# Optimization experiments

Measured on AMD Instinct MI355X. Metric: run time of the kernel, lower is better.

Reference implementation:

```python
import jax, jax.numpy as jnp
import numpy as np

I, H, B, T = 17, 128, 32768, 19

def setup_inputs() -> dict:
    key = jax.random.key(0)
    ks = jax.random.split(key, 7)
    s = 1.0 / np.sqrt(H)  # PyTorch LSTMCell/Linear init scale
    u = lambda k, shape: jax.random.uniform(k, shape, jnp.float32, -s, s)
    return {
        "x": jax.random.normal(ks[0], (B, T, I), jnp.float32),
        "W_ih": u(ks[1], (4 * H, I)),
        "W_hh": u(ks[2], (4 * H, H)),
        "b_ih": u(ks[3], (4 * H,)),
        "b_hh": u(ks[4], (4 * H,)),
        "W_out": u(ks[5], (I, H)),
        "b_out": u(ks[6], (I,)),
    }

def reference(x, W_ih, W_hh, b_ih, b_hh, W_out, b_out):
    B_, T_, _ = x.shape
    Hh = W_hh.shape[1]
    # Precompute input projections for all timesteps in one GEMM: [B,T,4H]
    x_proj = jnp.einsum('bti,gi->btg', x, W_ih) + b_ih + b_hh

    def step(carry, xp_t):
        h, c = carry
        gates = xp_t + h @ W_hh.T            # [B,4H]
        i_g, f_g, g_g, o_g = jnp.split(gates, 4, axis=-1)
        c = jax.nn.sigmoid(f_g) * c + jax.nn.sigmoid(i_g) * jnp.tanh(g_g)
        h = jax.nn.sigmoid(o_g) * jnp.tanh(c)
        y = h @ W_out.T + b_out              # [B,I]
        return (h, c), y

    h0 = jnp.zeros((B_, Hh), x.dtype)
    c0 = jnp.zeros((B_, Hh), x.dtype)
    _, ys = jax.lax.scan(step, (h0, c0), jnp.swapaxes(x_proj, 0, 1))  # ys: [T,B,I]
    return jnp.swapaxes(ys, 0, 1)  # [B,T,I]
```

## Files before the change

kernel.cpp:

```cpp
#include <hip/hip_runtime.h>

#define I_DIM 17
#define H_DIM 128
#define T_DIM 19
#define B_DIM 32768
#define M_ROWS 128
#define NTHR 512
#define GRID (B_DIM / M_ROWS)
#define XI 323
#define NF (M_ROWS * XI)
#define XSLOT 4352

#define OFF_H 0
#define OFF_X 65536
#define OFF_WO 148224
#define LDS_TOT 156416

typedef __bf16 bf16x8 __attribute__((ext_vector_type(8)));
typedef float f32x4 __attribute__((ext_vector_type(4)));
typedef float f32x4u __attribute__((ext_vector_type(4), aligned(4)));
union FragU { bf16x8 v; unsigned short s[8]; uint4 u; };

#define K1 1.4426950408889634f
#define K2 2.8853900817779268f

__device__ __forceinline__ unsigned short f2bf(float f) {
    union { float f; unsigned u; } x; x.f = f;
    return (unsigned short)((x.u + 0x8000u) >> 16);
}

#define SGB_STEP() do {                                        \
    _Pragma("unroll")                                          \
    for (int it_ = 0; it_ < 32; ++it_) {                       \
        __builtin_amdgcn_sched_group_barrier(0x100, 2, 0);     \
        __builtin_amdgcn_sched_group_barrier(0x008, 5, 0);     \
        __builtin_amdgcn_sched_group_barrier(0x002, 18, 0);    \
    }                                                          \
} while (0)

#define MFMA_Q(P_, QT_, ACC_, REC_) do {                                          \
    _Pragma("unroll") for (int m2 = 0; m2 < 2; ++m2) {                            \
        _Pragma("unroll") for (int g = 0; g < 4; ++g)                             \
            ACC_[m2][g] = bias[g];                                                \
        FragU fx; fx.u = (uint4){0u, 0u, 0u, 0u};                                 \
        if (q < 2)                                                                \
            fx.v = *(const bf16x8*)(smem + xyA + ((QT_) * 2 + m2) * 512);         \
        else if (q == 2)                                                          \
            fx.s[0] = *(const unsigned short*)(smem + xk16 + ((QT_) * 2 + m2) * 32); \
        _Pragma("unroll") for (int g = 0; g < 4; ++g)                             \
            ACC_[m2][g] = __builtin_amdgcn_mfma_f32_16x16x32_bf16(wihr[g], fx.v, ACC_[m2][g], 0, 0, 0); \
    }                                                                             \
    if (REC_) {                                                                   \
        _Pragma("unroll") for (int kk = 0; kk < 4; ++kk)                          \
            _Pragma("unroll") for (int m2 = 0; m2 < 2; ++m2) {                    \
                bf16x8 a = *(const bf16x8*)(smem + vkk[kk] + ((1 - (P_)) * 32768 + ((QT_) * 2 + m2) * 4096)); \
                _Pragma("unroll") for (int g = 0; g < 4; ++g)                     \
                    ACC_[m2][g] = __builtin_amdgcn_mfma_f32_16x16x32_bf16(whh[kk][g], a, ACC_[m2][g], 0, 0, 0); \
            }                                                                     \
    }                                                                             \
} while (0)

#define ELEM_Q(P_, QT_, ACC_) do {                                                \
    _Pragma("unroll") for (int m2 = 0; m2 < 2; ++m2) {                            \
        unsigned long long hp = 0ull;                                             \
        _Pragma("unroll") for (int r = 0; r < 4; ++r) {                           \
            float ui = __builtin_amdgcn_exp2f(ACC_[m2][0][r]);                    \
            float uf = __builtin_amdgcn_exp2f(ACC_[m2][1][r]);                    \
            float vg = __builtin_amdgcn_exp2f(ACC_[m2][2][r]);                    \
            float uo = __builtin_amdgcn_exp2f(ACC_[m2][3][r]);                    \
            float A_ = 1.f + ui, F_ = 1.f + uf, G_ = 1.f + vg;                    \
            float AG = A_ * G_;                                                   \
            int ci = (QT_) * 8 + m2 * 4 + r;                                      \
            float c = (cst[ci] * AG + (1.f - vg) * F_) * __builtin_amdgcn_rcpf(F_ * AG); \
            cst[ci] = c;                                                          \
            float vc = __builtin_amdgcn_exp2f(-K2 * c);                           \
            float h = (1.f - vc) * __builtin_amdgcn_rcpf((1.f + uo) * (1.f + vc));\
            union { float f; unsigned u; } hu; hu.f = h;                          \
            hp |= (unsigned long long)((hu.u + 0x8000u) >> 16) << (16 * r);       \
        }                                                                         \
        *(unsigned long long*)(smem + vwrT + ((P_) * 32768 + ((QT_) * 2 + m2) * 4096)) = hp; \
    }                                                                             \
} while (0)

#define Y_BURST(P_) do {                                                          \
    f32x4 ya0 = {0.f, 0.f, 0.f, 0.f}, ya1 = {0.f, 0.f, 0.f, 0.f};                 \
    _Pragma("unroll") for (int kk = 0; kk < 4; ++kk) {                            \
        bf16x8 wa = *(const bf16x8*)(smem + vwo + kk * 1024);                     \
        bf16x8 h0 = *(const bf16x8*)(smem + vkk[kk] + yrt + (1 - (P_)) * 32768);  \
        bf16x8 h1 = *(const bf16x8*)(smem + vkk[kk] + yrt + 4096 + (1 - (P_)) * 32768); \
        ya0 = __builtin_amdgcn_mfma_f32_16x16x32_bf16(wa, h0, ya0, 0, 0, 0);      \
        ya1 = __builtin_amdgcn_mfma_f32_16x16x32_bf16(wa, h1, ya1, 0, 0, 0);      \
    }                                                                             \
    if (yct == 0) {                                                               \
        *(f32x4u*)ypt0 = ya0 + ybo;                                               \
        *(f32x4u*)ypt1 = ya1 + ybo;                                               \
    } else if (q == 0) {                                                          \
        ypt0[0] = ya0[0] + ybo[0];                                                \
        ypt1[0] = ya1[0] + ybo[0];                                                \
    }                                                                             \
    ypt0 += I_DIM; ypt1 += I_DIM;                                                 \
} while (0)

#define STEP(P_) do {                      \
    MFMA_Q(P_, 0, accA, 1);                \
    MFMA_Q(P_, 1, accB, 1);                \
    ELEM_Q(P_, 0, accA);                   \
    MFMA_Q(P_, 2, accA, 1);                \
    ELEM_Q(P_, 1, accB);                   \
    MFMA_Q(P_, 3, accB, 1);                \
    ELEM_Q(P_, 2, accA);                   \
    Y_BURST(P_);                           \
    ELEM_Q(P_, 3, accB);                   \
    xyA += XSLOT; xk16 += XSLOT;           \
    SGB_STEP();                            \
    __syncthreads();                       \
} while (0)

__global__ __launch_bounds__(NTHR)
__attribute__((amdgpu_waves_per_eu(2, 2)))
void flowlstm(
    const float* __restrict__ x, const float* __restrict__ W_ih,
    const float* __restrict__ W_hh, const float* __restrict__ b_ih,
    const float* __restrict__ b_hh, const float* __restrict__ W_out,
    const float* __restrict__ b_out, float* __restrict__ out)
{
    __shared__ __align__(16) unsigned char smem[LDS_TOT];
    const int tid = threadIdx.x;
    const int w = tid >> 6, lane = tid & 63, l15 = lane & 15, q = lane >> 4;
    const int cg = w;
    const int b0 = blockIdx.x * M_ROWS;

    {
        const float* xb = x + (size_t)b0 * XI;
        for (int j = 0; j < 81; ++j) {
            int f = tid + j * NTHR;
            if (f < NF) {
                float v = xb[f];
                unsigned uf_ = (unsigned)f;
                unsigned row = (uf_ * 51943u) >> 24;
                unsigned s = uf_ - row * 323u;
                unsigned t = (s * 61681u) >> 20;
                unsigned k = s - t * 17u;
                unsigned a;
                if (k == 16) a = OFF_X + t * XSLOT + 4096 + row * 2;
                else a = OFF_X + t * XSLOT + (row >> 4) * 512 + (k >> 3) * 256
                       + (row & 15) * 16 + (k & 7) * 2;
                *(unsigned short*)(smem + a) = f2bf(v);
            }
        }
    }
    {
        int ln = tid & 63, f = tid >> 6;
        int kk = f & 3, ct = f >> 2;
        int o = ct * 16 + (ln & 15);
        int kb = kk * 32 + (ln >> 4) * 8;
        FragU fu;
        #pragma unroll
        for (int e = 0; e < 8; ++e)
            fu.s[e] = (o < I_DIM) ? f2bf(W_out[o * H_DIM + kb + e]) : (unsigned short)0;
        *(uint4*)(smem + OFF_WO + f * 1024 + ln * 16) = fu.u;
    }
    float gsc[4] = { -K1, -K1, -K2, -K1 };

    bf16x8 whh[4][4];
    #pragma unroll
    for (int kk = 0; kk < 4; ++kk)
        #pragma unroll
        for (int g = 0; g < 4; ++g) {
            int n = g * H_DIM + cg * 16 + l15;
            const float* s = W_hh + n * H_DIM + kk * 32 + q * 8;
            FragU fu;
            #pragma unroll
            for (int e = 0; e < 8; ++e) fu.s[e] = f2bf(s[e] * gsc[g]);
            whh[kk][g] = fu.v;
        }
    bf16x8 wihr[4];
    #pragma unroll
    for (int g = 0; g < 4; ++g) {
        int n = g * H_DIM + cg * 16 + l15;
        FragU fu;
        #pragma unroll
        for (int e = 0; e < 8; ++e) {
            int k = q * 8 + e;
            fu.s[e] = (k < I_DIM) ? f2bf(W_ih[n * I_DIM + k] * gsc[g]) : (unsigned short)0;
        }
        wihr[g] = fu.v;
    }
    f32x4 bias[4];
    #pragma unroll
    for (int g = 0; g < 4; ++g)
        #pragma unroll
        for (int r = 0; r < 4; ++r) {
            int col = g * H_DIM + cg * 16 + 4 * q + r;
            bias[g][r] = (b_ih[col] + b_hh[col]) * gsc[g];
        }
    const unsigned xr7 = (unsigned)((l15 & 7) << 4);
    unsigned vkk[4];
    #pragma unroll
    for (int kk = 0; kk < 4; ++kk)
        vkk[kk] = (unsigned)(l15 * 256 + ((kk * 64 + q * 16) ^ xr7));
    const unsigned vwrT = (unsigned)(l15 * 256 + (((cg * 16 + 4 * q) * 2) ^ xr7));
    const int yct = w & 1;
    const unsigned yrt = (unsigned)((w >> 1) * 8192);
    const unsigned vwo = (unsigned)(OFF_WO + yct * 4096 + lane * 16);
    f32x4 ybo;
    #pragma unroll
    for (int r = 0; r < 4; ++r) {
        int col = yct * 16 + 4 * q + r;
        ybo[r] = b_out[col < I_DIM ? col : 16];
    }
    unsigned xyA  = (unsigned)(OFF_X + (q < 2 ? q * 256 : 0) + l15 * 16);
    unsigned xk16 = (unsigned)(OFF_X + 4096 + l15 * 2);
    float* ypt0 = out + (size_t)(b0 + (w >> 1) * 32 + l15) * XI + (yct ? 16 : 4 * q);
    float* ypt1 = ypt0 + (size_t)16 * XI;

    float cst[32];
    #pragma unroll
    for (int i = 0; i < 32; ++i) cst[i] = 0.f;

    f32x4 accA[2][4], accB[2][4];

    __syncthreads();

    MFMA_Q(0, 0, accA, 0);
    MFMA_Q(0, 1, accB, 0);
    ELEM_Q(0, 0, accA);
    MFMA_Q(0, 2, accA, 0);
    ELEM_Q(0, 1, accB);
    MFMA_Q(0, 3, accB, 0);
    ELEM_Q(0, 2, accA);
    ELEM_Q(0, 3, accB);
    xyA += XSLOT; xk16 += XSLOT;
    __syncthreads();

    #pragma unroll 1
    for (int t = 1; t < T_DIM; t += 2) {
        STEP(1);
        STEP(0);
    }

    {
        f32x4 ya0 = {0.f, 0.f, 0.f, 0.f}, ya1 = {0.f, 0.f, 0.f, 0.f};
        #pragma unroll
        for (int kk = 0; kk < 4; ++kk) {
            bf16x8 wa = *(const bf16x8*)(smem + vwo + kk * 1024);
            bf16x8 h0 = *(const bf16x8*)(smem + vkk[kk] + yrt);
            bf16x8 h1 = *(const bf16x8*)(smem + vkk[kk] + yrt + 4096);
            ya0 = __builtin_amdgcn_mfma_f32_16x16x32_bf16(wa, h0, ya0, 0, 0, 0);
            ya1 = __builtin_amdgcn_mfma_f32_16x16x32_bf16(wa, h1, ya1, 0, 0, 0);
        }
        if (yct == 0) {
            *(f32x4u*)ypt0 = ya0 + ybo;
            *(f32x4u*)ypt1 = ya1 + ybo;
        } else if (q == 0) {
            ypt0[0] = ya0[0] + ybo[0];
            ypt1[0] = ya1[0] + ybo[0];
        }
    }
}

extern "C" void kernel_launch(void* const* d_in, const int* in_sizes, int n_in,
                              void* d_out, int out_size, void* d_ws, size_t ws_size,
                              hipStream_t stream) {
    const float* x     = (const float*)d_in[0];
    const float* W_ih  = (const float*)d_in[1];
    const float* W_hh  = (const float*)d_in[2];
    const float* b_ih  = (const float*)d_in[3];
    const float* b_hh  = (const float*)d_in[4];
    const float* W_out = (const float*)d_in[5];
    const float* b_out = (const float*)d_in[6];
    float* out = (float*)d_out;

    dim3 grid(GRID), block(NTHR);
    flowlstm<<<grid, block, 0, stream>>>(x, W_ih, W_hh, b_ih, b_hh, W_out, b_out, out);
}
```

Measured before the change: 150.0 us.

## Split batch tile into two half-groups and ping-pong LSTM steps between them

Splits the 128-row block into two 64-row groups with separate h buffers in LDS (GB0/GB1) and interleaves them: while one group's elementwise gate math runs, the other group's MFMA recurrence is issued. This replaces double-buffering h over time, which shrinks the LDS footprint, and drops the explicit sched_group_barrier scheduling hints. The intent is to overlap the transcendental VALU work with matrix-core work across independent batch halves. The cost is two barriers per timestep instead of one, and instruction ordering now depends on the compiler's default scheduling.

```diff
diff --git a/kernel.cpp b/kernel.cpp
--- a/kernel.cpp
+++ b/kernel.cpp
@@ -11,10 +11,11 @@
 #define NF (M_ROWS * XI)
 #define XSLOT 4352
 
-#define OFF_H 0
-#define OFF_X 65536
-#define OFF_WO 148224
-#define LDS_TOT 156416
+#define GB0 0
+#define GB1 16384
+#define OFF_X 32768
+#define OFF_WO 115456
+#define LDS_TOT 123648
 
 typedef __bf16 bf16x8 __attribute__((ext_vector_type(8)));
 typedef float f32x4 __attribute__((ext_vector_type(4)));
@@ -29,91 +30,57 @@
     return (unsigned short)((x.u + 0x8000u) >> 16);
 }
 
-#define SGB_STEP() do {                                        \
-    _Pragma("unroll")                                          \
-    for (int it_ = 0; it_ < 32; ++it_) {                       \
-        __builtin_amdgcn_sched_group_barrier(0x100, 2, 0);     \
-        __builtin_amdgcn_sched_group_barrier(0x008, 5, 0);     \
-        __builtin_amdgcn_sched_group_barrier(0x002, 18, 0);    \
-    }                                                          \
+#define MFMA_Q(QT_, GB_, XB_, XK_, REC_) do {                                     \
+    _Pragma("unroll") for (int g = 0; g < 4; ++g)                                 \
+        acc[QT_][g] = bias[g];                                                    \
+    FragU fx; fx.u = (uint4){0u, 0u, 0u, 0u};                                     \
+    if (q < 2)                                                                    \
+        fx.v = *(const bf16x8*)(smem + (XB_) + (QT_) * 512);                      \
+    else if (q == 2)                                                              \
+        fx.s[0] = *(const unsigned short*)(smem + (XK_) + (QT_) * 32);            \
+    _Pragma("unroll") for (int g = 0; g < 4; ++g)                                 \
+        acc[QT_][g] = __builtin_amdgcn_mfma_f32_16x16x32_bf16(wihr[g], fx.v, acc[QT_][g], 0, 0, 0); \
+    if (REC_) {                                                                   \
+        _Pragma("unroll") for (int kk = 0; kk < 4; ++kk) {                        \
+            bf16x8 a = *(const bf16x8*)(smem + vkk[kk] + ((GB_) + (QT_) * 4096)); \
+            _Pragma("unroll") for (int g = 0; g < 4; ++g)                         \
+                acc[QT_][g] = __builtin_amdgcn_mfma_f32_16x16x32_bf16(whh[kk][g], a, acc[QT_][g], 0, 0, 0); \
+        }                                                                         \
+    }                                                                             \
 } while (0)
 
-#define MFMA_Q(P_, QT_, ACC_, REC_) do {                                          \
-    _Pragma("unroll") for (int m2 = 0; m2 < 2; ++m2) {                            \
-        _Pragma("unroll") for (int g = 0; g < 4; ++g)                             \
-            ACC_[m2][g] = bias[g];                                                \
-        FragU fx; fx.u = (uint4){0u, 0u, 0u, 0u};                                 \
-        if (q < 2)                                                                \
-            fx.v = *(const bf16x8*)(smem + xyA + ((QT_) * 2 + m2) * 512);         \
-        else if (q == 2)                                                          \
-            fx.s[0] = *(const unsigned short*)(smem + xk16 + ((QT_) * 2 + m2) * 32); \
-        _Pragma("unroll") for (int g = 0; g < 4; ++g)                             \
-            ACC_[m2][g] = __builtin_amdgcn_mfma_f32_16x16x32_bf16(wihr[g], fx.v, ACC_[m2][g], 0, 0, 0); \
-    }                                                                             \
-    if (REC_) {                                                                   \
-        _Pragma("unroll") for (int kk = 0; kk < 4; ++kk)                          \
-            _Pragma("unroll") for (int m2 = 0; m2 < 2; ++m2) {                    \
-                bf16x8 a = *(const bf16x8*)(smem + vkk[kk] + ((1 - (P_)) * 32768 + ((QT_) * 2 + m2) * 4096)); \
-                _Pragma("unroll") for (int g = 0; g < 4; ++g)                     \
-                    ACC_[m2][g] = __builtin_amdgcn_mfma_f32_16x16x32_bf16(whh[kk][g], a, ACC_[m2][g], 0, 0, 0); \
-            }                                                                     \
-    }                                                                             \
+#define ELEM_Q(QT_, GB_, CST_) do {                                               \
+    unsigned long long hp = 0ull;                                                 \
+    _Pragma("unroll") for (int r = 0; r < 4; ++r) {                               \
+        float ui = __builtin_amdgcn_exp2f(acc[QT_][0][r]);                        \
+        float uf = __builtin_amdgcn_exp2f(acc[QT_][1][r]);                        \
+        float vg = __builtin_amdgcn_exp2f(acc[QT_][2][r]);                        \
+        float uo = __builtin_amdgcn_exp2f(acc[QT_][3][r]);                        \
+        float A_ = 1.f + ui, F_ = 1.f + uf, G_ = 1.f + vg;                        \
+        float AG = A_ * G_;                                                       \
+        int ci = (QT_) * 4 + r;                                                   \
+        float c = (CST_[ci] * AG + (1.f - vg) * F_) * __builtin_amdgcn_rcpf(F_ * AG); \
+        CST_[ci] = c;                                                             \
+        float vc = __builtin_amdgcn_exp2f(-K2 * c);                               \
+        float h = (1.f - vc) * __builtin_amdgcn_rcpf((1.f + uo) * (1.f + vc));    \
+        union { float f; unsigned u; } hu; hu.f = h;                              \
+        hp |= (unsigned long long)((hu.u + 0x8000u) >> 16) << (16 * r);           \
+    }                                                                             \
+    *(unsigned long long*)(smem + vwrT + ((GB_) + (QT_) * 4096)) = hp;            \
 } while (0)
 
-#define ELEM_Q(P_, QT_, ACC_) do {                                                \
-    _Pragma("unroll") for (int m2 = 0; m2 < 2; ++m2) {                            \
-        unsigned long long hp = 0ull;                                             \
-        _Pragma("unroll") for (int r = 0; r < 4; ++r) {                           \
-            float ui = __builtin_amdgcn_exp2f(ACC_[m2][0][r]);                    \
-            float uf = __builtin_amdgcn_exp2f(ACC_[m2][1][r]);                    \
-            float vg = __builtin_amdgcn_exp2f(ACC_[m2][2][r]);                    \
-            float uo = __builtin_amdgcn_exp2f(ACC_[m2][3][r]);                    \
-            float A_ = 1.f + ui, F_ = 1.f + uf, G_ = 1.f + vg;                    \
-            float AG = A_ * G_;                                                   \
-            int ci = (QT_) * 8 + m2 * 4 + r;                                      \
-            float c = (cst[ci] * AG + (1.f - vg) * F_) * __builtin_amdgcn_rcpf(F_ * AG); \
-            cst[ci] = c;                                                          \
-            float vc = __builtin_amdgcn_exp2f(-K2 * c);                           \
-            float h = (1.f - vc) * __builtin_amdgcn_rcpf((1.f + uo) * (1.f + vc));\
-            union { float f; unsigned u; } hu; hu.f = h;                          \
-            hp |= (unsigned long long)((hu.u + 0x8000u) >> 16) << (16 * r);       \
-        }                                                                         \
-        *(unsigned long long*)(smem + vwrT + ((P_) * 32768 + ((QT_) * 2 + m2) * 4096)) = hp; \
-    }                                                                             \
-} while (0)
-
-#define Y_BURST(P_) do {                                                          \
-    f32x4 ya0 = {0.f, 0.f, 0.f, 0.f}, ya1 = {0.f, 0.f, 0.f, 0.f};                 \
+#define Y_T(GB_, YP_) do {                                                        \
+    f32x4 ya = {0.f, 0.f, 0.f, 0.f};                                              \
     _Pragma("unroll") for (int kk = 0; kk < 4; ++kk) {                            \
         bf16x8 wa = *(const bf16x8*)(smem + vwo + kk * 1024);                     \
-        bf16x8 h0 = *(const bf16x8*)(smem + vkk[kk] + yrt + (1 - (P_)) * 32768);  \
-        bf16x8 h1 = *(const bf16x8*)(smem + vkk[kk] + yrt + 4096 + (1 - (P_)) * 32768); \
-        ya0 = __builtin_amdgcn_mfma_f32_16x16x32_bf16(wa, h0, ya0, 0, 0, 0);      \
-        ya1 = __builtin_amdgcn_mfma_f32_16x16x32_bf16(wa, h1, ya1, 0, 0, 0);      \
+        bf16x8 hb = *(const bf16x8*)(smem + vkk[kk] + ((GB_) + 0) + yrt4);        \
+        ya = __builtin_amdgcn_mfma_f32_16x16x32_bf16(wa, hb, ya, 0, 0, 0);        \
     }                                                                             \
     if (yct == 0) {                                                               \
-        *(f32x4u*)ypt0 = ya0 + ybo;                                               \
-        *(f32x4u*)ypt1 = ya1 + ybo;                                               \
+        *(f32x4u*)(YP_) = ya + ybo;                                               \
     } else if (q == 0) {                                                          \
-        ypt0[0] = ya0[0] + ybo[0];                                                \
-        ypt1[0] = ya1[0] + ybo[0];                                                \
-    }                                                                             \
-    ypt0 += I_DIM; ypt1 += I_DIM;                                                 \
-} while (0)
-
-#define STEP(P_) do {                      \
-    MFMA_Q(P_, 0, accA, 1);                \
-    MFMA_Q(P_, 1, accB, 1);                \
-    ELEM_Q(P_, 0, accA);                   \
-    MFMA_Q(P_, 2, accA, 1);                \
-    ELEM_Q(P_, 1, accB);                   \
-    MFMA_Q(P_, 3, accB, 1);                \
-    ELEM_Q(P_, 2, accA);                   \
-    Y_BURST(P_);                           \
-    ELEM_Q(P_, 3, accB);                   \
-    xyA += XSLOT; xk16 += XSLOT;           \
-    SGB_STEP();                            \
-    __syncthreads();                       \
+        (YP_)[0] = ya[0] + ybo[0];                                                \
+    }                                                                             \
 } while (0)
 
 __global__ __launch_bounds__(NTHR)
@@ -201,7 +168,7 @@
         vkk[kk] = (unsigned)(l15 * 256 + ((kk * 64 + q * 16) ^ xr7));
     const unsigned vwrT = (unsigned)(l15 * 256 + (((cg * 16 + 4 * q) * 2) ^ xr7));
     const int yct = w & 1;
-    const unsigned yrt = (unsigned)((w >> 1) * 8192);
+    const unsigned yrt4 = (unsigned)((w >> 1) * 4096);
     const unsigned vwo = (unsigned)(OFF_WO + yct * 4096 + lane * 16);
     f32x4 ybo;
     #pragma unroll
@@ -211,52 +178,54 @@
     }
     unsigned xyA  = (unsigned)(OFF_X + (q < 2 ? q * 256 : 0) + l15 * 16);
     unsigned xk16 = (unsigned)(OFF_X + 4096 + l15 * 2);
-    float* ypt0 = out + (size_t)(b0 + (w >> 1) * 32 + l15) * XI + (yct ? 16 : 4 * q);
-    float* ypt1 = ypt0 + (size_t)16 * XI;
-
-    float cst[32];
-    #pragma unroll
-    for (int i = 0; i < 32; ++i) cst[i] = 0.f;
-
-    f32x4 accA[2][4], accB[2][4];
-
-    __syncthreads();
-
-    MFMA_Q(0, 0, accA, 0);
-    MFMA_Q(0, 1, accB, 0);
-    ELEM_Q(0, 0, accA);
-    MFMA_Q(0, 2, accA, 0);
-    ELEM_Q(0, 1, accB);
-    MFMA_Q(0, 3, accB, 0);
-    ELEM_Q(0, 2, accA);
-    ELEM_Q(0, 3, accB);
+    float* ypG0 = out + (size_t)(b0 + (w >> 1) * 16 + l15) * XI + (yct ? 16 : 4 * q);
+    float* ypG1 = ypG0 + (size_t)64 * XI;
+
+    float cstA[16], cstB[16];
+    #pragma unroll
+    for (int i = 0; i < 16; ++i) { cstA[i] = 0.f; cstB[i] = 0.f; }
+
+    f32x4 acc[4][4];
+
+    __syncthreads();
+
+    MFMA_Q(0, GB0, xyA, xk16, 0);
+    MFMA_Q(1, GB0, xyA, xk16, 0);
+    MFMA_Q(2, GB0, xyA, xk16, 0);
+    MFMA_Q(3, GB0, xyA, xk16, 0);
+    __syncthreads();
+    ELEM_Q(0, GB0, cstA); MFMA_Q(0, GB1, xyA + 2048, xk16 + 128, 0);
+    ELEM_Q(1, GB0, cstA); MFMA_Q(1, GB1, xyA + 2048, xk16 + 128, 0);
+    ELEM_Q(2, GB0, cstA); MFMA_Q(2, GB1, xyA + 2048, xk16 + 128, 0);
+    ELEM_Q(3, GB0, cstA); MFMA_Q(3, GB1, xyA + 2048, xk16 + 128, 0);
+    __syncthreads();
     xyA += XSLOT; xk16 += XSLOT;
-    __syncthreads();
 
     #pragma unroll 1
-    for (int t = 1; t < T_DIM; t += 2) {
-        STEP(1);
-        STEP(0);
-    }
-
-    {
-        f32x4 ya0 = {0.f, 0.f, 0.f, 0.f}, ya1 = {0.f, 0.f, 0.f, 0.f};
-        #pragma unroll
-        for (int kk = 0; kk < 4; ++kk) {
-            bf16x8 wa = *(const bf16x8*)(smem + vwo + kk * 1024);
-            bf16x8 h0 = *(const bf16x8*)(smem + vkk[kk] + yrt);
-            bf16x8 h1 = *(const bf16x8*)(smem + vkk[kk] + yrt + 4096);
-            ya0 = __builtin_amdgcn_mfma_f32_16x16x32_bf16(wa, h0, ya0, 0, 0, 0);
-            ya1 = __builtin_amdgcn_mfma_f32_16x16x32_bf16(wa, h1, ya1, 0, 0, 0);
-        }
-        if (yct == 0) {
-            *(f32x4u*)ypt0 = ya0 + ybo;
-            *(f32x4u*)ypt1 = ya1 + ybo;
-        } else if (q == 0) {
-            ypt0[0] = ya0[0] + ybo[0];
-            ypt1[0] = ya1[0] + ybo[0];
-        }
-    }
+    for (int k = 1; k < T_DIM; ++k) {
+        ELEM_Q(0, GB1, cstB); MFMA_Q(0, GB0, xyA, xk16, 1);
+        ELEM_Q(1, GB1, cstB); MFMA_Q(1, GB0, xyA, xk16, 1);
+        Y_T(GB0, ypG0);
+        ELEM_Q(2, GB1, cstB); MFMA_Q(2, GB0, xyA, xk16, 1);
+        ELEM_Q(3, GB1, cstB); MFMA_Q(3, GB0, xyA, xk16, 1);
+        __syncthreads();
+        ELEM_Q(0, GB0, cstA); MFMA_Q(0, GB1, xyA + 2048, xk16 + 128, 1);
+        ELEM_Q(1, GB0, cstA); MFMA_Q(1, GB1, xyA + 2048, xk16 + 128, 1);
+        Y_T(GB1, ypG1);
+        ELEM_Q(2, GB0, cstA); MFMA_Q(2, GB1, xyA + 2048, xk16 + 128, 1);
+        ELEM_Q(3, GB0, cstA); MFMA_Q(3, GB1, xyA + 2048, xk16 + 128, 1);
+        __syncthreads();
+        xyA += XSLOT; xk16 += XSLOT;
+        ypG0 += I_DIM; ypG1 += I_DIM;
+    }
+
+    ELEM_Q(0, GB1, cstB);
+    ELEM_Q(1, GB1, cstB);
+    Y_T(GB0, ypG0);
+    ELEM_Q(2, GB1, cstB);
+    ELEM_Q(3, GB1, cstB);
+    __syncthreads();
+    Y_T(GB1, ypG1);
 }
 
 extern "C" void kernel_launch(void* const* d_in, const int* in_sizes, int n_in,
```

Result: no change. 151.1 us (+0.7%).
